# Optimization experiments

Hardware: AMD Instinct MI355X
Metric: run time of the kernel (lower is better)

Reference implementation:

```python
import jax, jax.numpy as jnp
import numpy as np

B, T, F, H = 128, 256, 64, 512


def _lstm_cell(x, h, c, Wih, Whh, bih, bhh):
    # PyTorch gate order: i, f, g, o
    g = x @ Wih.T + h @ Whh.T + bih + bhh  # [B, 4H]
    i, f, gg, o = jnp.split(g, 4, axis=-1)
    i = jax.nn.sigmoid(i)
    f = jax.nn.sigmoid(f)
    gg = jnp.tanh(gg)
    o = jax.nn.sigmoid(o)
    c = f * c + i * gg
    h = o * jnp.tanh(c)
    return h, c


def setup_inputs() -> dict:
    key = jax.random.key(0)
    ks = jax.random.split(key, 20)
    s = lambda k, shp: (jax.random.normal(k, shp, jnp.float32) * 0.05)
    return {
        "x": jax.random.normal(ks[0], (B, T, F), jnp.float32),
        # encoder LSTM (2 layers)
        "enc_Wih0": s(ks[1], (4 * H, F)), "enc_Whh0": s(ks[2], (4 * H, H)),
        "enc_bih0": s(ks[3], (4 * H,)), "enc_bhh0": s(ks[4], (4 * H,)),
        "enc_Wih1": s(ks[5], (4 * H, H)), "enc_Whh1": s(ks[6], (4 * H, H)),
        "enc_bih1": s(ks[7], (4 * H,)), "enc_bhh1": s(ks[8], (4 * H,)),
        # decoder LSTM (2 layers)
        "dec_Wih0": s(ks[9], (4 * H, F)), "dec_Whh0": s(ks[10], (4 * H, H)),
        "dec_bih0": s(ks[11], (4 * H,)), "dec_bhh0": s(ks[12], (4 * H,)),
        "dec_Wih1": s(ks[13], (4 * H, H)), "dec_Whh1": s(ks[14], (4 * H, H)),
        "dec_bih1": s(ks[15], (4 * H,)), "dec_bhh1": s(ks[16], (4 * H,)),
        # decoder output projection
        "lin_W": s(ks[17], (F, H)), "lin_b": s(ks[18], (F,)),
    }


def reference(x, enc_Wih0, enc_Whh0, enc_bih0, enc_bhh0,
              enc_Wih1, enc_Whh1, enc_bih1, enc_bhh1,
              dec_Wih0, dec_Whh0, dec_bih0, dec_bhh0,
              dec_Wih1, dec_Whh1, dec_bih1, dec_bhh1,
              lin_W, lin_b):
    b, t, f = x.shape
    zeros = jnp.zeros((b, H), x.dtype)

    # ---- encoder: stacked 2-layer LSTM over time, keep only final (h, c) ----
    def enc_step(carry, xt):
        h0, c0, h1, c1 = carry
        h0, c0 = _lstm_cell(xt, h0, c0, enc_Wih0, enc_Whh0, enc_bih0, enc_bhh0)
        h1, c1 = _lstm_cell(h0, h1, c1, enc_Wih1, enc_Whh1, enc_bih1, enc_bhh1)
        return (h0, c0, h1, c1), None

    (h0, c0, h1, c1), _ = jax.lax.scan(enc_step, (zeros, zeros, zeros, zeros),
                                       jnp.swapaxes(x, 0, 1))  # [T, B, F]

    def dec_step(carry, _):
        xin, h0, c0, h1, c1 = carry
        h0, c0 = _lstm_cell(xin, h0, c0, dec_Wih0, dec_Whh0, dec_bih0, dec_bhh0)
        h1, c1 = _lstm_cell(h0, h1, c1, dec_Wih1, dec_Whh1, dec_bih1, dec_bhh1)
        out = h1 @ lin_W.T + lin_b  # [B, F]
        return (out, h0, c0, h1, c1), out

    x_last = x[:, -1, :]
    _, ys = jax.lax.scan(dec_step, (x_last, h0, c0, h1, c1), None, length=t)
    # generated step j fills output index t-1-j -> reverse time axis
    return jnp.flip(jnp.swapaxes(ys, 0, 1), axis=1)  # [B, T, F]
```

## Files before the change

kernel.cpp:

```cpp
#include <hip/hip_runtime.h>
#include <math.h>

#define T_ 256
#define H_ 512
#define NWG 256
#define NTHR 256
#define WPG 64

typedef _Float16 half8 __attribute__((ext_vector_type(8)));
typedef float f32x4 __attribute__((ext_vector_type(4)));
typedef unsigned short u16;
typedef unsigned int u32;
typedef unsigned long long u64;

#define O_H0R  0u
#define O_H1R  2097152u
#define O_BAR  4194304u

#define E0W 0u
#define E1W 36864u
#define D0W 0u
#define D1W 65536u

__device__ __forceinline__ float sigf(float x) { return 1.0f / (1.0f + expf(-x)); }

__device__ __forceinline__ u16 f2h_bits(float f) {
    _Float16 h = (_Float16)f;
    return __builtin_bit_cast(u16, h);
}
__device__ __forceinline__ float h2f(u16 x) {
    return (float)__builtin_bit_cast(_Float16, x);
}

__device__ __forceinline__ void llc_store64(u64* p, u64 v) {
    __hip_atomic_store(p, v, __ATOMIC_RELAXED, __HIP_MEMORY_SCOPE_AGENT);
}
__device__ __forceinline__ void llc_store32(u32* p, u32 v) {
    __hip_atomic_store(p, v, __ATOMIC_RELAXED, __HIP_MEMORY_SCOPE_AGENT);
}

__device__ __forceinline__ void gbar_arrive(int* flags, int w, int gen) {
    asm volatile("s_waitcnt vmcnt(0)" ::: "memory");
    __syncthreads();
    if (threadIdx.x == 0)
        __hip_atomic_store(flags + w * 16, gen, __ATOMIC_RELAXED, __HIP_MEMORY_SCOPE_AGENT);
}
__device__ __forceinline__ void gbar_wait(int* flags, int gbase, int gen, bool inv) {
    if (threadIdx.x < 64) {
        while (__hip_atomic_load(flags + (gbase + threadIdx.x) * 16,
                                 __ATOMIC_RELAXED, __HIP_MEMORY_SCOPE_AGENT) < gen)
            __builtin_amdgcn_s_sleep(1);
    }
    __syncthreads();
    if (inv) {
        if (threadIdx.x == 0) __builtin_amdgcn_fence(__ATOMIC_ACQUIRE, "agent");
        __syncthreads();
    }
}

__device__ __forceinline__ void st_w(char* smem, unsigned base, unsigned K2,
                                     unsigned m, unsigned k, float v) {
    _Float16 hh = (_Float16)v;
    unsigned off = (m * K2 + k * 2) ^ ((m & 7) << 4);
    *(u16*)(smem + base + off) = __builtin_bit_cast(u16, hh);
}

__device__ __forceinline__ void load_plane(uint4 (&buf)[16], const u32* __restrict__ plane,
                                           unsigned loff) {
    #pragma unroll
    for (int i = 0; i < 16; ++i)
        buf[i] = *(const uint4*)(plane + (size_t)i * 2048 + loff);
}

__device__ __forceinline__ void cons_plane(const uint4 (&buf)[16], const char* __restrict__ smem,
                                           unsigned base, unsigned K2, unsigned wk0,
                                           unsigned R, unsigned qq, f32x4& acc) {
    const unsigned swz = (R & 7) << 4;
    #pragma unroll
    for (int i = 0; i < 16; ++i) {
        const unsigned wb = R * K2 + (wk0 + (unsigned)i * 32 + qq * 8) * 2;
        half8 av = *(const half8*)(smem + base + (wb ^ swz));
        half8 bv = __builtin_bit_cast(half8, buf[i]);
        acc = __builtin_amdgcn_mfma_f32_16x16x32_f16(av, bv, acc, 0, 0, 0);
    }
}

__device__ __forceinline__ void seg_x(
    const char* smem, unsigned base, unsigned K2,
    const float* __restrict__ x, int t, unsigned bt, unsigned R, int lane, f32x4& acc) {
    const unsigned mm = lane & 15, qq = lane >> 4;
    const unsigned swz = (R & 7) << 4;
    const float* xp = x + ((size_t)(bt + mm) * T_ + t) * 64 + qq * 8;
    #pragma unroll
    for (int i = 0; i < 2; ++i) {
        float4 f0 = *(const float4*)(xp + i * 32);
        float4 f1 = *(const float4*)(xp + i * 32 + 4);
        float fs[8] = { f0.x, f0.y, f0.z, f0.w, f1.x, f1.y, f1.z, f1.w };
        half8 bv;
        #pragma unroll
        for (int j = 0; j < 8; ++j) bv[j] = (_Float16)fs[j];
        unsigned wb = (R * K2 + (qq * 8 + i * 32) * 2) ^ swz;
        half8 av = *(const half8*)(smem + base + wb);
        acc = __builtin_amdgcn_mfma_f32_16x16x32_f16(av, bv, acc, 0, 0, 0);
    }
}

__device__ __forceinline__ void epilogue_reg(f32x4 acc, const float* bz, int u, int b,
                                             float& cr, u32* hw, int lane) {
    float gi = sigf(acc[0] + bz[0]);
    float gf = sigf(acc[1] + bz[1]);
    float gt = tanhf(acc[2] + bz[2]);
    float go = sigf(acc[3] + bz[3]);
    float cn = gf * cr + gi * gt;
    cr = cn;
    float hv = go * tanhf(cn);
    u16 mybits = f2h_bits(hv);
    int other = __shfl_xor((int)(u32)mybits, 16);
    if (((lane >> 4) & 1) == 0) {
        u32 pk = (u32)mybits | (((u32)other & 0xFFFFu) << 16);
        unsigned idx = (unsigned)(u >> 5) * 2048 + (unsigned)b * 16 + ((unsigned)(u & 31) >> 1);
        llc_store32(hw + idx, pk);
    }
}

__device__ __forceinline__ void linear_out(const u32* __restrict__ h1p,
                                           const float* __restrict__ linW,
                                           const float* __restrict__ linb,
                                           float* __restrict__ out, int g, int wl,
                                           int tid, int t) {
    const int bl = g * 32 + (wl >> 1);
    const int kq = tid & 7;
    const int f  = (wl & 1) * 32 + (tid >> 3);
    float s = 0.f;
    #pragma unroll
    for (int c2 = 0; c2 < 2; ++c2) {
        const int ch = kq * 2 + c2;
        const u64* ph = (const u64*)h1p + (size_t)ch * 1024 + (size_t)bl * 8;
        const float* wp = linW + (size_t)f * H_ + ch * 32;
        #pragma unroll
        for (int j = 0; j < 8; ++j) {
            u64 r = ph[j];
            s += h2f((u16)r)         * wp[4 * j + 0];
            s += h2f((u16)(r >> 16)) * wp[4 * j + 1];
            s += h2f((u16)(r >> 32)) * wp[4 * j + 2];
            s += h2f((u16)(r >> 48)) * wp[4 * j + 3];
        }
    }
    s += __shfl_xor(s, 1);
    s += __shfl_xor(s, 2);
    s += __shfl_xor(s, 4);
    if (kq == 0)
        out[((size_t)bl * T_ + (255 - t)) * 64 + f] = s + linb[f];
}

__global__ __launch_bounds__(NTHR, 1) void lstm_persist(
    const float* __restrict__ x,
    const float* __restrict__ eWih0, const float* __restrict__ eWhh0,
    const float* __restrict__ ebih0, const float* __restrict__ ebhh0,
    const float* __restrict__ eWih1, const float* __restrict__ eWhh1,
    const float* __restrict__ ebih1, const float* __restrict__ ebhh1,
    const float* __restrict__ dWih0, const float* __restrict__ dWhh0,
    const float* __restrict__ dbih0, const float* __restrict__ dbhh0,
    const float* __restrict__ dWih1, const float* __restrict__ dWhh1,
    const float* __restrict__ dbih1, const float* __restrict__ dbhh1,
    const float* __restrict__ linW,  const float* __restrict__ linb,
    float* __restrict__ out, char* __restrict__ wsb, int* __restrict__ flags) {
    extern __shared__ char smem[];
    const int w = blockIdx.x, tid = threadIdx.x;
    const int lane = tid & 63, wave = tid >> 6;

    const int g = w >> 6;
    const int wl = w & 63;
    const int gbase = g * WPG;
    const int u_base = wl * 8;
    const int mh = wave >> 1;
    const int bh = wave & 1;
    const int u = u_base + mh * 4 + (lane >> 4);
    const unsigned bt = (unsigned)(g * 32 + bh * 16);
    const int b = (int)bt + (lane & 15);
    const unsigned R = (unsigned)(mh * 16 + (lane & 15));
    const unsigned qq = (unsigned)(lane >> 4);
    const unsigned loff = (bt + (unsigned)(lane & 15)) * 16 + qq * 4;

    #define H0S(t) ((u32*)(wsb + O_H0R + (unsigned)((t) & 15) * 131072u))
    #define H1S(t) ((u32*)(wsb + O_H1R + (unsigned)((t) & 15) * 131072u))
    int gen = 0;

    {
        const int gtid = wl * NTHR + tid;
        if (gtid < 12288) {
            const int slot  = gtid >> 12;
            const int rem   = gtid & 4095;
            const int chunk = rem >> 8;
            const int brow  = (rem & 255) >> 3;
            const int q     = rem & 7;
            u64* base = (slot == 0) ? (u64*)(wsb + O_H0R + 15u * 131072u)
                      : (slot == 1) ? (u64*)(wsb + O_H1R + 14u * 131072u)
                                    : (u64*)(wsb + O_H1R + 15u * 131072u);
            llc_store64(base + (size_t)chunk * 1024 + (size_t)(g * 32 + brow) * 8 + q, 0ULL);
        }
    }
    float bzA[4], bzB[4], bzD0[4], bzD0b[4], bzD1[4];
    #pragma unroll
    for (int gg = 0; gg < 4; ++gg) {
        const int gr = gg * H_ + u;
        bzA[gg] = ebih0[gr] + ebhh0[gr];
        bzB[gg] = ebih1[gr] + ebhh1[gr];
        float d0 = dbih0[gr] + dbhh0[gr];
        bzD0[gg] = d0;
        float s = 0.f;
        for (int f = 0; f < 64; ++f) s += dWih0[(size_t)gr * 64 + f] * linb[f];
        bzD0b[gg] = d0 + s;
        bzD1[gg] = dbih1[gr] + dbhh1[gr];
    }
    float c0r = 0.f, c1r = 0.f;

    for (int mr = 0; mr < 32; ++mr) {
        const int gr = (mr & 3) * H_ + u_base + (mr >> 2);
        for (int k = tid; k < 576; k += NTHR) {
            float v = (k < 64) ? eWih0[(size_t)gr * 64 + k] : eWhh0[(size_t)gr * H_ + (k - 64)];
            st_w(smem, E0W, 1152, mr, k, v);
        }
        for (int k = tid; k < 1024; k += NTHR) {
            float v = (k < 512) ? eWih1[(size_t)gr * H_ + k] : eWhh1[(size_t)gr * H_ + (k - 512)];
            st_w(smem, E1W, 2048, mr, k, v);
        }
    }
    gbar_arrive(flags, w, ++gen);
    gbar_wait(flags, gbase, gen, false);

    uint4 P[16], Q[16];

    for (int p = 0; p <= T_; ++p) {
        gbar_arrive(flags, w, ++gen);
        f32x4 a = {0,0,0,0}, e = {0,0,0,0};
        if (p < T_) seg_x(smem, E0W, 1152, x, p, bt, R, lane, a);
        gbar_wait(flags, gbase, gen, p > 0 && (p & 15) == 0);
        load_plane(P, H0S(p - 1), loff);
        if (p >= 1) load_plane(Q, H1S(p - 2), loff);
        if (p < T_) cons_plane(P, smem, E0W, 1152, 64, R, qq, a);
        if (p >= 1) {
            cons_plane(P, smem, E1W, 2048, 0,   R, qq, e);
            cons_plane(Q, smem, E1W, 2048, 512, R, qq, e);
        }
        if (p < T_)  epilogue_reg(a, bzA, u, b, c0r, H0S(p), lane);
        if (p >= 1)  epilogue_reg(e, bzB, u, b, c1r, H1S(p - 1), lane);
    }

    __syncthreads();
    for (int mr = 0; mr < 32; ++mr) {
        const int gr = (mr & 3) * H_ + u_base + (mr >> 2);
        const float* wr = dWih0 + (size_t)gr * 64;
        for (int c = tid; c < 512; c += NTHR) {
            float s = 0.f;
            #pragma unroll 8
            for (int f = 0; f < 64; ++f) s += wr[f] * linW[(size_t)f * H_ + c];
            st_w(smem, D0W, 2048, mr, c, s);
            st_w(smem, D0W, 2048, mr, 512 + c, dWhh0[(size_t)gr * H_ + c]);
            st_w(smem, D1W, 2048, mr, c,       dWih1[(size_t)gr * H_ + c]);
            st_w(smem, D1W, 2048, mr, 512 + c, dWhh1[(size_t)gr * H_ + c]);
        }
    }
    __syncthreads();

    for (int t = 0; t < T_; ++t) {
        {
            gbar_arrive(flags, w, ++gen);
            f32x4 a = {0,0,0,0};
            if (t > 0) {
                cons_plane(Q, smem, D0W, 2048, 512, R, qq, a);
            } else {
                const float* xr = x + ((size_t)b * T_ + (T_ - 1)) * 64;
                #pragma unroll
                for (int gg = 0; gg < 4; ++gg) {
                    const float* wr = dWih0 + (size_t)(gg * H_ + u) * 64;
                    float s = 0.f;
                    for (int f = 0; f < 64; ++f) s += wr[f] * xr[f];
                    a[gg] = s;
                }
            }
            gbar_wait(flags, gbase, gen, t > 0 && (t & 15) == 0);
            if (t > 0) {
                load_plane(P, H1S(t - 1), loff);
                cons_plane(P, smem, D0W, 2048, 0, R, qq, a);
            } else {
                load_plane(Q, H0S(-1), loff);
                cons_plane(Q, smem, D0W, 2048, 512, R, qq, a);
            }
            epilogue_reg(a, (t > 0) ? bzD0b : bzD0, u, b, c0r, H0S(t), lane);
            if (t > 0) linear_out(H1S(t - 1), linW, linb, out, g, wl, tid, t - 1);
        }
        {
            gbar_arrive(flags, w, ++gen);
            f32x4 e = {0,0,0,0};
            if (t > 0)
                cons_plane(P, smem, D1W, 2048, 512, R, qq, e);
            gbar_wait(flags, gbase, gen, false);
            load_plane(Q, H0S(t), loff);
            if (t == 0) {
                load_plane(P, H1S(-1), loff);
                cons_plane(P, smem, D1W, 2048, 512, R, qq, e);
            }
            cons_plane(Q, smem, D1W, 2048, 0, R, qq, e);
            epilogue_reg(e, bzD1, u, b, c1r, H1S(t), lane);
        }
    }
    asm volatile("s_waitcnt vmcnt(0)" ::: "memory");
    __syncthreads();
    linear_out(H1S(255), linW, linb, out, g, wl, tid, 255);
}

extern "C" void kernel_launch(void* const* d_in, const int* in_sizes, int n_in,
                              void* d_out, int out_size, void* d_ws, size_t ws_size,
                              hipStream_t stream) {
    (void)in_sizes; (void)n_in; (void)out_size; (void)ws_size;
    const float* x     = (const float*)d_in[0];
    const float* eWih0 = (const float*)d_in[1];
    const float* eWhh0 = (const float*)d_in[2];
    const float* ebih0 = (const float*)d_in[3];
    const float* ebhh0 = (const float*)d_in[4];
    const float* eWih1 = (const float*)d_in[5];
    const float* eWhh1 = (const float*)d_in[6];
    const float* ebih1 = (const float*)d_in[7];
    const float* ebhh1 = (const float*)d_in[8];
    const float* dWih0 = (const float*)d_in[9];
    const float* dWhh0 = (const float*)d_in[10];
    const float* dbih0 = (const float*)d_in[11];
    const float* dbhh0 = (const float*)d_in[12];
    const float* dWih1 = (const float*)d_in[13];
    const float* dWhh1 = (const float*)d_in[14];
    const float* dbih1 = (const float*)d_in[15];
    const float* dbhh1 = (const float*)d_in[16];
    const float* linW  = (const float*)d_in[17];
    const float* linb  = (const float*)d_in[18];

    char* wsb  = (char*)d_ws;
    int* flags = (int*)(wsb + O_BAR);

    static const int lds_bytes = 131072;
    hipFuncSetAttribute((const void*)lstm_persist,
                        hipFuncAttributeMaxDynamicSharedMemorySize, lds_bytes);

    hipMemsetAsync(flags, 0, NWG * 64, stream);

    hipLaunchKernelGGL(lstm_persist, dim3(NWG), dim3(NTHR), lds_bytes, stream,
                       x, eWih0, eWhh0, ebih0, ebhh0, eWih1, eWhh1, ebih1, ebhh1,
                       dWih0, dWhh0, dbih0, dbhh0, dWih1, dWhh1, dbih1, dbhh1,
                       linW, linb, (float*)d_out, wsb, flags);
}
```

Before: 3.716 ms.

## Deepen encoder layer-1 pipeline and move decoder output projection off critical path

The encoder wavefront pipeline now lags layer 1 by two steps. This lets the h0 input contribution for layer 1 be computed from the previous step's registers before the grid barrier instead of after it. In the decoder, the output linear projection moves into the pre-barrier slot of the second half-step, overlapping it with barrier waiting. The acquire fence now runs on every barrier rather than every 16th step, and the final projection is guarded by a full grid barrier. This adds a cache invalidate per step, one extra encoder iteration and 16 extra registers.

```diff
diff --git a/kernel.cpp b/kernel.cpp
--- a/kernel.cpp
+++ b/kernel.cpp
@@ -45,17 +45,15 @@
     if (threadIdx.x == 0)
         __hip_atomic_store(flags + w * 16, gen, __ATOMIC_RELAXED, __HIP_MEMORY_SCOPE_AGENT);
 }
-__device__ __forceinline__ void gbar_wait(int* flags, int gbase, int gen, bool inv) {
+__device__ __forceinline__ void gbar_wait(int* flags, int gbase, int gen) {
     if (threadIdx.x < 64) {
         while (__hip_atomic_load(flags + (gbase + threadIdx.x) * 16,
                                  __ATOMIC_RELAXED, __HIP_MEMORY_SCOPE_AGENT) < gen)
             __builtin_amdgcn_s_sleep(1);
     }
     __syncthreads();
-    if (inv) {
-        if (threadIdx.x == 0) __builtin_amdgcn_fence(__ATOMIC_ACQUIRE, "agent");
-        __syncthreads();
-    }
+    if (threadIdx.x == 0) __builtin_amdgcn_fence(__ATOMIC_ACQUIRE, "agent");
+    __syncthreads();
 }
 
 __device__ __forceinline__ void st_w(char* smem, unsigned base, unsigned K2,
@@ -227,24 +225,26 @@
         }
     }
     gbar_arrive(flags, w, ++gen);
-    gbar_wait(flags, gbase, gen, false);
-
-    uint4 P[16], Q[16];
-
-    for (int p = 0; p <= T_; ++p) {
+    gbar_wait(flags, gbase, gen);
+
+    uint4 P[16], Q[16], Pprev[16];
+
+    for (int p = 0; p <= T_ + 1; ++p) {
         gbar_arrive(flags, w, ++gen);
         f32x4 a = {0,0,0,0}, e = {0,0,0,0};
-        if (p < T_) seg_x(smem, E0W, 1152, x, p, bt, R, lane, a);
-        gbar_wait(flags, gbase, gen, p > 0 && (p & 15) == 0);
-        load_plane(P, H0S(p - 1), loff);
-        if (p >= 1) load_plane(Q, H1S(p - 2), loff);
-        if (p < T_) cons_plane(P, smem, E0W, 1152, 64, R, qq, a);
-        if (p >= 1) {
-            cons_plane(P, smem, E1W, 2048, 0,   R, qq, e);
+        if (p < T_)  seg_x(smem, E0W, 1152, x, p, bt, R, lane, a);
+        if (p >= 2)  cons_plane(Pprev, smem, E1W, 2048, 0, R, qq, e);
+        gbar_wait(flags, gbase, gen);
+        if (p <= T_) load_plane(P, H0S(p - 1), loff);
+        if (p < T_)  cons_plane(P, smem, E0W, 1152, 64, R, qq, a);
+        if (p >= 2) {
+            load_plane(Q, H1S(p - 3), loff);
             cons_plane(Q, smem, E1W, 2048, 512, R, qq, e);
         }
         if (p < T_)  epilogue_reg(a, bzA, u, b, c0r, H0S(p), lane);
-        if (p >= 1)  epilogue_reg(e, bzB, u, b, c1r, H1S(p - 1), lane);
+        if (p >= 2)  epilogue_reg(e, bzB, u, b, c1r, H1S(p - 2), lane);
+        #pragma unroll
+        for (int i = 0; i < 16; ++i) Pprev[i] = P[i];
     }
 
     __syncthreads();
@@ -279,7 +279,7 @@
                     a[gg] = s;
                 }
             }
-            gbar_wait(flags, gbase, gen, t > 0 && (t & 15) == 0);
+            gbar_wait(flags, gbase, gen);
             if (t > 0) {
                 load_plane(P, H1S(t - 1), loff);
                 cons_plane(P, smem, D0W, 2048, 0, R, qq, a);
@@ -288,14 +288,15 @@
                 cons_plane(Q, smem, D0W, 2048, 512, R, qq, a);
             }
             epilogue_reg(a, (t > 0) ? bzD0b : bzD0, u, b, c0r, H0S(t), lane);
-            if (t > 0) linear_out(H1S(t - 1), linW, linb, out, g, wl, tid, t - 1);
         }
         {
             gbar_arrive(flags, w, ++gen);
             f32x4 e = {0,0,0,0};
-            if (t > 0)
+            if (t > 0) {
                 cons_plane(P, smem, D1W, 2048, 512, R, qq, e);
-            gbar_wait(flags, gbase, gen, false);
+                linear_out(H1S(t - 1), linW, linb, out, g, wl, tid, t - 1);
+            }
+            gbar_wait(flags, gbase, gen);
             load_plane(Q, H0S(t), loff);
             if (t == 0) {
                 load_plane(P, H1S(-1), loff);
@@ -305,8 +306,8 @@
             epilogue_reg(e, bzD1, u, b, c1r, H1S(t), lane);
         }
     }
-    asm volatile("s_waitcnt vmcnt(0)" ::: "memory");
-    __syncthreads();
+    gbar_arrive(flags, w, ++gen);
+    gbar_wait(flags, gbase, gen);
     linear_out(H1S(255), linW, linb, out, g, wl, tid, 255);
 }
 
```

Result: slower. 4.374 ms (+17.7%).
